# Performance work log

Measured on AMD Instinct MI355X. Metric: run time of the kernel, lower is better.

The kernel has to match this reference:

```python
import jax, jax.numpy as jnp
import numpy as np

B_BOXES = 5
N_CLASSES = 80
LAMBDA_COORD = 5.0
LAMBDA_NOOBJ = 0.5
LAMBDA_CLASS = 1.0
EPS = 1e-6


def _corners(b):
    # b: (..., 4) center-format (x, y, w, h) -> x1, y1, x2, y2
    x, y, w, h = b[..., 0], b[..., 1], b[..., 2], b[..., 3]
    return x - w / 2, y - h / 2, x + w / 2, y + h / 2


def pairwise_iou(p_box, t_box):
    # p_box, t_box: (N, S, S, B, 4) -> ious: (N, S, S, B_pred, B_tgt)
    px1, py1, px2, py2 = _corners(p_box[..., :, None, :])
    tx1, ty1, tx2, ty2 = _corners(t_box[..., None, :, :])
    iw = jnp.clip(jnp.minimum(px2, tx2) - jnp.maximum(px1, tx1), 0.0)
    ih = jnp.clip(jnp.minimum(py2, ty2) - jnp.maximum(py1, ty1), 0.0)
    inter = iw * ih
    area_p = (px2 - px1) * (py2 - py1)
    area_t = (tx2 - tx1) * (ty2 - ty1)
    return inter / (area_p + area_t - inter + EPS)


def setup_inputs() -> dict:
    key = jax.random.key(0)
    k1, k2 = jax.random.split(key)
    N, S = 128, 26
    ch = B_BOXES * (5 + N_CLASSES)  # 425
    preds = jax.random.normal(k1, (N, S, S, ch), dtype=jnp.float32)
    targets = jax.random.normal(k2, (N, S, S, ch), dtype=jnp.float32)
    return {"preds": preds, "targets": targets}


def reference(preds, targets):
    N, S = preds.shape[0], preds.shape[1]
    D = 5 + N_CLASSES
    p = preds.reshape(N, S, S, B_BOXES, D)
    t = targets.reshape(N, S, S, B_BOXES, D)

    ious = pairwise_iou(p[..., :4], t[..., :4])          # (N,S,S,B,B)
    best = jnp.argmax(ious, axis=-1)                      # (N,S,S,B)
    idx = jnp.broadcast_to(best[..., None], t.shape)
    matched = jnp.take_along_axis(t, idx, axis=3)         # (N,S,S,B,D)

    obj = (matched[..., 4] > 0).astype(p.dtype)           # (N,S,S,B)
    noobj = 1.0 - obj

    xy_loss = LAMBDA_COORD * jnp.sum(obj[..., None] * (p[..., 0:2] - matched[..., 0:2]) ** 2)

    pwh = jnp.sqrt(jnp.abs(p[..., 2:4] + EPS))
    twh = jnp.sqrt(jnp.abs(matched[..., 2:4] + EPS))
    wh_loss = LAMBDA_COORD * jnp.sum(obj[..., None] * (pwh - twh) ** 2)

    conf_sq = (p[..., 4] - matched[..., 4]) ** 2
    conf_loss_obj = jnp.sum(obj * conf_sq)
    conf_loss_noobj = LAMBDA_NOOBJ * jnp.sum(noobj * conf_sq)

    tcls = jnp.argmax(t[..., 5:], axis=-1)                # (N,S,S,B)
    logp = jax.nn.log_softmax(p[..., 5:], axis=-1)
    nll = -jnp.take_along_axis(logp, tcls[..., None], axis=-1)[..., 0]
    class_loss = LAMBDA_CLASS * jnp.sum(obj * nll)

    return xy_loss + wh_loss + conf_loss_obj + conf_loss_noobj + class_loss
```

## Files before the change

### kernel.cpp

```cpp
#include <hip/hip_runtime.h>
#include <math.h>

#define NB 5
#define NC 80
#define DD 85
#define CH 425
#define EPSF 1e-6f
#define CPB 51
#define TPB 256

__device__ __forceinline__ void load5(const float* __restrict__ arr, int idx,
                                      float& a, float& b, float& c, float& d, float& e)
{
    const int a0 = idx & ~3;
    const int r  = idx & 3;
    const float4 u = *(const float4*)(arr + a0);
    const float4 v = *(const float4*)(arr + a0 + 4);
    switch (r) {
    case 0:  a = u.x; b = u.y; c = u.z; d = u.w; e = v.x; break;
    case 1:  a = u.y; b = u.z; c = u.w; d = v.x; e = v.y; break;
    case 2:  a = u.z; b = u.w; c = v.x; d = v.y; e = v.z; break;
    default: a = u.w; b = v.x; c = v.y; d = v.z; e = v.w; break;
    }
}

__global__ __launch_bounds__(TPB) void yolo_loss_kernel(
    const float* __restrict__ preds,
    const float* __restrict__ targets,
    float* __restrict__ out,
    int ncells)
{
    __shared__ float s_pb[CPB * NB * 5];
    __shared__ float s_tb[CPB * NB * 5];
    __shared__ float s_nll[CPB * NB];
    __shared__ float s_wsum[4];

    const int tid   = threadIdx.x;
    const int cell0 = blockIdx.x * CPB;
    const int cells = min(CPB, ncells - cell0);
    const int nt    = cells * NB;

    if (tid < nt) {
        const int c = tid / 5;
        const int b = tid - c * 5;
        const int g = (cell0 + c) * CH + b * DD;
        float a0, a1, a2, a3, a4;
        load5(preds, g, a0, a1, a2, a3, a4);
        float* d = s_pb + tid * 5;
        d[0] = a0; d[1] = a1; d[2] = a2; d[3] = a3; d[4] = a4;
        load5(targets, g, a0, a1, a2, a3, a4);
        d = s_tb + tid * 5;
        d[0] = a0; d[1] = a1; d[2] = a2; d[3] = a3; d[4] = a4;
    }

    {
        const int grp  = tid >> 4;
        const int lane = tid & 15;
        #pragma unroll
        for (int r = 0; r < 16; ++r) {
            const int t = r * 16 + grp;
            if (t < nt) {
                const int c = t / 5;
                const int b = t - c * 5;
                const int g = (cell0 + c) * CH + b * DD + 5 + lane;
                float s  = 0.0f;
                float bv = -INFINITY;
                int   bi = 0x7fffffff;
                float bp = 0.0f;
                #pragma unroll
                for (int k = 0; k < 5; ++k) {
                    const float pl = preds[g + 16 * k];
                    const float tl = targets[g + 16 * k];
                    s += __expf(pl);
                    if (tl > bv) { bv = tl; bi = lane + 16 * k; bp = pl; }
                }
                #pragma unroll
                for (int m = 1; m < 16; m <<= 1) {
                    s += __shfl_xor(s, m, 16);
                    const float ov = __shfl_xor(bv, m, 16);
                    const int   oi = __shfl_xor(bi, m, 16);
                    const float op = __shfl_xor(bp, m, 16);
                    if (ov > bv || (ov == bv && oi < bi)) { bv = ov; bi = oi; bp = op; }
                }
                if (lane == 0) s_nll[t] = __logf(s) - bp;
            }
        }
    }

    __syncthreads();

    float acc = 0.0f;
    if (tid < nt) {
        const int c = tid / 5;
        const float* P = s_pb + tid * 5;
        const float px = P[0], py = P[1], pw = P[2], ph = P[3], pconf = P[4];
        const float px1 = px - pw * 0.5f, py1 = py - ph * 0.5f;
        const float px2 = px + pw * 0.5f, py2 = py + ph * 0.5f;
        const float area_p = (px2 - px1) * (py2 - py1);

        float best = -INFINITY;
        float mx = 0.f, my = 0.f, mw = 0.f, mh = 0.f, mconf = 0.f;
        #pragma unroll
        for (int j = 0; j < NB; ++j) {
            const float* T = s_tb + (c * 5 + j) * 5;
            const float tx = T[0], ty = T[1], tw = T[2], th = T[3], tcf = T[4];
            const float tx1 = tx - tw * 0.5f, ty1 = ty - th * 0.5f;
            const float tx2 = tx + tw * 0.5f, ty2 = ty + th * 0.5f;
            float iw = fminf(px2, tx2) - fmaxf(px1, tx1); iw = fmaxf(iw, 0.0f);
            float ih = fminf(py2, ty2) - fmaxf(py1, ty1); ih = fmaxf(ih, 0.0f);
            const float inter  = iw * ih;
            const float area_t = (tx2 - tx1) * (ty2 - ty1);
            const float iou    = inter / (area_p + area_t - inter + EPSF);
            if (iou > best) { best = iou; mx = tx; my = ty; mw = tw; mh = th; mconf = tcf; }
        }

        const float obj = (mconf > 0.0f) ? 1.0f : 0.0f;
        const float dx = px - mx, dy = py - my;
        float term = 5.0f * obj * (dx * dx + dy * dy);
        const float dw = sqrtf(fabsf(pw + EPSF)) - sqrtf(fabsf(mw + EPSF));
        const float dh = sqrtf(fabsf(ph + EPSF)) - sqrtf(fabsf(mh + EPSF));
        term += 5.0f * obj * (dw * dw + dh * dh);
        const float dc  = pconf - mconf;
        const float csq = dc * dc;
        term += obj * csq + 0.5f * (1.0f - obj) * csq;
        term += obj * s_nll[tid];
        acc = term;
    }

    #pragma unroll
    for (int off = 32; off > 0; off >>= 1) acc += __shfl_down(acc, off, 64);
    if ((tid & 63) == 0) s_wsum[tid >> 6] = acc;
    __syncthreads();
    if (tid == 0) {
        atomicAdd(out, s_wsum[0] + s_wsum[1] + s_wsum[2] + s_wsum[3]);
    }
}

extern "C" void kernel_launch(void* const* d_in, const int* in_sizes, int n_in,
                              void* d_out, int out_size, void* d_ws, size_t ws_size,
                              hipStream_t stream) {
    const float* preds   = (const float*)d_in[0];
    const float* targets = (const float*)d_in[1];
    float* out = (float*)d_out;

    const int ncells = in_sizes[0] / CH;
    const int blocks = (ncells + CPB - 1) / CPB;

    hipMemsetAsync(out, 0, sizeof(float), stream);
    yolo_loss_kernel<<<blocks, TPB, 0, stream>>>(preds, targets, out, ncells);
}
```

Measured before the change: 315.1 us.

## Stage full cell chunks in LDS with coalesced float4 loads, pairwise class reduction

Each block now copies a contiguous chunk of 16 cells of preds and targets into shared memory using coalesced float4 loads. The class log-softmax and argmax are then computed from LDS by two threads per box, replacing the strided 16-lane global reads. The change aims to cut scattered global access and make the memory stream fully coalesced. In exchange it uses more LDS per block, leaves most threads idle during compute, and assumes the cell count divides evenly by 16 with no tail handling.

```diff
diff --git a/kernel.cpp b/kernel.cpp
--- a/kernel.cpp
+++ b/kernel.cpp
@@ -6,125 +6,102 @@
 #define DD 85
 #define CH 425
 #define EPSF 1e-6f
-#define CPB 51
+#define CPB 16
+#define CHUNK_F (CPB * CH)
+#define CHUNK_F4 (CHUNK_F / 4)
 #define TPB 256
-
-__device__ __forceinline__ void load5(const float* __restrict__ arr, int idx,
-                                      float& a, float& b, float& c, float& d, float& e)
-{
-    const int a0 = idx & ~3;
-    const int r  = idx & 3;
-    const float4 u = *(const float4*)(arr + a0);
-    const float4 v = *(const float4*)(arr + a0 + 4);
-    switch (r) {
-    case 0:  a = u.x; b = u.y; c = u.z; d = u.w; e = v.x; break;
-    case 1:  a = u.y; b = u.z; c = u.w; d = v.x; e = v.y; break;
-    case 2:  a = u.z; b = u.w; c = v.x; d = v.y; e = v.z; break;
-    default: a = u.w; b = v.x; c = v.y; d = v.z; e = v.w; break;
-    }
-}
+#define NITER 7
 
 __global__ __launch_bounds__(TPB) void yolo_loss_kernel(
     const float* __restrict__ preds,
     const float* __restrict__ targets,
-    float* __restrict__ out,
-    int ncells)
+    float* __restrict__ out)
 {
-    __shared__ float s_pb[CPB * NB * 5];
-    __shared__ float s_tb[CPB * NB * 5];
-    __shared__ float s_nll[CPB * NB];
+    __shared__ float4 s_p4[CHUNK_F4];
+    __shared__ float4 s_t4[CHUNK_F4];
     __shared__ float s_wsum[4];
+    const float* sp = (const float*)s_p4;
+    const float* st = (const float*)s_t4;
 
-    const int tid   = threadIdx.x;
-    const int cell0 = blockIdx.x * CPB;
-    const int cells = min(CPB, ncells - cell0);
-    const int nt    = cells * NB;
+    const int tid = threadIdx.x;
+    const long long g0 = (long long)blockIdx.x * CHUNK_F;
+    const float4* gp = (const float4*)(preds + g0);
+    const float4* gt = (const float4*)(targets + g0);
 
-    if (tid < nt) {
-        const int c = tid / 5;
-        const int b = tid - c * 5;
-        const int g = (cell0 + c) * CH + b * DD;
-        float a0, a1, a2, a3, a4;
-        load5(preds, g, a0, a1, a2, a3, a4);
-        float* d = s_pb + tid * 5;
-        d[0] = a0; d[1] = a1; d[2] = a2; d[3] = a3; d[4] = a4;
-        load5(targets, g, a0, a1, a2, a3, a4);
-        d = s_tb + tid * 5;
-        d[0] = a0; d[1] = a1; d[2] = a2; d[3] = a3; d[4] = a4;
+    float4 rp[NITER], rt[NITER];
+    #pragma unroll
+    for (int j = 0; j < NITER; ++j) {
+        const int idx = tid + j * TPB;
+        if (idx < CHUNK_F4) { rp[j] = gp[idx]; rt[j] = gt[idx]; }
     }
-
-    {
-        const int grp  = tid >> 4;
-        const int lane = tid & 15;
-        #pragma unroll
-        for (int r = 0; r < 16; ++r) {
-            const int t = r * 16 + grp;
-            if (t < nt) {
-                const int c = t / 5;
-                const int b = t - c * 5;
-                const int g = (cell0 + c) * CH + b * DD + 5 + lane;
-                float s  = 0.0f;
-                float bv = -INFINITY;
-                int   bi = 0x7fffffff;
-                float bp = 0.0f;
-                #pragma unroll
-                for (int k = 0; k < 5; ++k) {
-                    const float pl = preds[g + 16 * k];
-                    const float tl = targets[g + 16 * k];
-                    s += __expf(pl);
-                    if (tl > bv) { bv = tl; bi = lane + 16 * k; bp = pl; }
-                }
-                #pragma unroll
-                for (int m = 1; m < 16; m <<= 1) {
-                    s += __shfl_xor(s, m, 16);
-                    const float ov = __shfl_xor(bv, m, 16);
-                    const int   oi = __shfl_xor(bi, m, 16);
-                    const float op = __shfl_xor(bp, m, 16);
-                    if (ov > bv || (ov == bv && oi < bi)) { bv = ov; bi = oi; bp = op; }
-                }
-                if (lane == 0) s_nll[t] = __logf(s) - bp;
-            }
-        }
+    #pragma unroll
+    for (int j = 0; j < NITER; ++j) {
+        const int idx = tid + j * TPB;
+        if (idx < CHUNK_F4) { s_p4[idx] = rp[j]; s_t4[idx] = rt[j]; }
     }
-
     __syncthreads();
 
     float acc = 0.0f;
-    if (tid < nt) {
-        const int c = tid / 5;
-        const float* P = s_pb + tid * 5;
-        const float px = P[0], py = P[1], pw = P[2], ph = P[3], pconf = P[4];
-        const float px1 = px - pw * 0.5f, py1 = py - ph * 0.5f;
-        const float px2 = px + pw * 0.5f, py2 = py + ph * 0.5f;
-        const float area_p = (px2 - px1) * (py2 - py1);
+    if (tid < 2 * CPB * NB) {
+        const int t = tid >> 1;
+        const int h = tid & 1;
+        const int kb = t * DD + 5 + h * 40;
+        float s  = 0.0f;
+        float bv = -INFINITY;
+        int   bi = 0x7fffffff;
+        float bp = 0.0f;
+        #pragma unroll 8
+        for (int k = 0; k < 40; ++k) {
+            const float pl = sp[kb + k];
+            const float tl = st[kb + k];
+            s += __expf(pl);
+            if (tl > bv) { bv = tl; bi = h * 40 + k; bp = pl; }
+        }
+        s += __shfl_xor(s, 1, 64);
+        const float ov = __shfl_xor(bv, 1, 64);
+        const int   oi = __shfl_xor(bi, 1, 64);
+        const float op = __shfl_xor(bp, 1, 64);
+        if (ov > bv || (ov == bv && oi < bi)) { bv = ov; bi = oi; bp = op; }
+        const float nll = __logf(s) - bp;
 
-        float best = -INFINITY;
-        float mx = 0.f, my = 0.f, mw = 0.f, mh = 0.f, mconf = 0.f;
-        #pragma unroll
-        for (int j = 0; j < NB; ++j) {
-            const float* T = s_tb + (c * 5 + j) * 5;
-            const float tx = T[0], ty = T[1], tw = T[2], th = T[3], tcf = T[4];
-            const float tx1 = tx - tw * 0.5f, ty1 = ty - th * 0.5f;
-            const float tx2 = tx + tw * 0.5f, ty2 = ty + th * 0.5f;
-            float iw = fminf(px2, tx2) - fmaxf(px1, tx1); iw = fmaxf(iw, 0.0f);
-            float ih = fminf(py2, ty2) - fmaxf(py1, ty1); ih = fmaxf(ih, 0.0f);
-            const float inter  = iw * ih;
-            const float area_t = (tx2 - tx1) * (ty2 - ty1);
-            const float iou    = inter / (area_p + area_t - inter + EPSF);
-            if (iou > best) { best = iou; mx = tx; my = ty; mw = tw; mh = th; mconf = tcf; }
+        if (h == 0) {
+            const int c = t / 5;
+            const int pb = t * DD;
+            const float px = sp[pb + 0], py = sp[pb + 1], pw = sp[pb + 2],
+                        ph = sp[pb + 3], pconf = sp[pb + 4];
+            const float px1 = px - pw * 0.5f, py1 = py - ph * 0.5f;
+            const float px2 = px + pw * 0.5f, py2 = py + ph * 0.5f;
+            const float area_p = (px2 - px1) * (py2 - py1);
+
+            float best = -INFINITY;
+            float mx = 0.f, my = 0.f, mw = 0.f, mh = 0.f, mconf = 0.f;
+            #pragma unroll
+            for (int j = 0; j < NB; ++j) {
+                const int tb = c * CH + j * DD;
+                const float tx = st[tb + 0], ty = st[tb + 1], tw = st[tb + 2],
+                            th = st[tb + 3], tcf = st[tb + 4];
+                const float tx1 = tx - tw * 0.5f, ty1 = ty - th * 0.5f;
+                const float tx2 = tx + tw * 0.5f, ty2 = ty + th * 0.5f;
+                float iw = fminf(px2, tx2) - fmaxf(px1, tx1); iw = fmaxf(iw, 0.0f);
+                float ih = fminf(py2, ty2) - fmaxf(py1, ty1); ih = fmaxf(ih, 0.0f);
+                const float inter  = iw * ih;
+                const float area_t = (tx2 - tx1) * (ty2 - ty1);
+                const float iou    = inter / (area_p + area_t - inter + EPSF);
+                if (iou > best) { best = iou; mx = tx; my = ty; mw = tw; mh = th; mconf = tcf; }
+            }
+
+            const float obj = (mconf > 0.0f) ? 1.0f : 0.0f;
+            const float dx = px - mx, dy = py - my;
+            float term = 5.0f * obj * (dx * dx + dy * dy);
+            const float dw = sqrtf(fabsf(pw + EPSF)) - sqrtf(fabsf(mw + EPSF));
+            const float dh = sqrtf(fabsf(ph + EPSF)) - sqrtf(fabsf(mh + EPSF));
+            term += 5.0f * obj * (dw * dw + dh * dh);
+            const float dc  = pconf - mconf;
+            const float csq = dc * dc;
+            term += obj * csq + 0.5f * (1.0f - obj) * csq;
+            term += obj * nll;
+            acc = term;
         }
-
-        const float obj = (mconf > 0.0f) ? 1.0f : 0.0f;
-        const float dx = px - mx, dy = py - my;
-        float term = 5.0f * obj * (dx * dx + dy * dy);
-        const float dw = sqrtf(fabsf(pw + EPSF)) - sqrtf(fabsf(mw + EPSF));
-        const float dh = sqrtf(fabsf(ph + EPSF)) - sqrtf(fabsf(mh + EPSF));
-        term += 5.0f * obj * (dw * dw + dh * dh);
-        const float dc  = pconf - mconf;
-        const float csq = dc * dc;
-        term += obj * csq + 0.5f * (1.0f - obj) * csq;
-        term += obj * s_nll[tid];
-        acc = term;
     }
 
     #pragma unroll
@@ -144,8 +121,8 @@
     float* out = (float*)d_out;
 
     const int ncells = in_sizes[0] / CH;
-    const int blocks = (ncells + CPB - 1) / CPB;
+    const int blocks = ncells / CPB;
 
     hipMemsetAsync(out, 0, sizeof(float), stream);
-    yolo_loss_kernel<<<blocks, TPB, 0, stream>>>(preds, targets, out, ncells);
+    yolo_loss_kernel<<<blocks, TPB, 0, stream>>>(preds, targets, out);
 }
```

Measured after the change: 368.0 us. +16.8%, slower.
